# Kernel optimization log

Hardware: AMD Instinct MI355X
Metric: run time of the kernel (lower is better)

The kernel has to match this reference:

```python
import jax, jax.numpy as jnp
import numpy as np

B, S, H, F, E, K, R = 1, 1024, 1024, 4096, 8, 2, 16
SCALING = 2.0  # lora_alpha / lora_r = 32 / 16


def setup_inputs() -> dict:
    key = jax.random.key(0)
    ks = jax.random.split(key, 14)
    rnd = lambda i, shape, scale=0.02: (jax.random.normal(ks[i], shape, jnp.float32) * scale)
    return {
        "hidden_states": rnd(0, (B, S, H), 1.0),
        "noise": rnd(1, (B * S, E), 1.0),          # stands in for torch.randn_like(logits)
        "w_route": rnd(2, (H, E)),                   # gate.topkroute_linear.weight^T
        "w_noise": rnd(3, (H, E)),                   # gate.noise_linear.weight^T
        "w_gate": rnd(4, (H, F)),                    # shared mlp gate_proj
        "w_up": rnd(5, (H, F)),                      # shared mlp up_proj
        "w_down": rnd(6, (F, H)),                    # shared mlp down_proj
        "a_gate": rnd(7, (E, H, R)),                 # per-expert LoRA A/B on gate_proj
        "b_gate": rnd(8, (E, R, F)),
        "a_up": rnd(9, (E, H, R)),
        "b_up": rnd(10, (E, R, F)),
        "a_down": rnd(11, (E, F, R)),
        "b_down": rnd(12, (E, R, H)),
    }


def reference(hidden_states, noise, w_route, w_noise, w_gate, w_up, w_down,
              a_gate, b_gate, a_up, b_up, a_down, b_down):
    Bx, Sx, Hx = hidden_states.shape
    x = hidden_states.reshape(-1, Hx)                       # [T, H]
    T = x.shape[0]

    # NoisyTopkRouter
    logits = x @ w_route                                     # [T, E]
    noise_logits = x @ w_noise
    router_logits = logits + noise * jax.nn.softplus(noise_logits)

    # softmax in fp32, top-k, renormalize
    probs = jax.nn.softmax(router_logits.astype(jnp.float32), axis=-1)
    rw, sel = jax.lax.top_k(probs, K)                        # [T, K]
    rw = rw / rw.sum(axis=-1, keepdims=True)
    rw = rw.astype(x.dtype)

    # dense per-(token, expert) combine weights (equiv. to the gather/index_add loop)
    wdense = jnp.zeros((T, E), x.dtype).at[jnp.arange(T)[:, None], sel].add(rw)  # [T, E]

    # LoRA experts (Mixtral MLP shared `mlp` + per-expert low-rank adapters), vectorized over E
    gate = jnp.einsum('th,hf->tf', x, w_gate)[None] + SCALING * jnp.einsum('th,ehr,erf->etf', x, a_gate, b_gate)  # [E,T,F]
    up = jnp.einsum('th,hf->tf', x, w_up)[None] + SCALING * jnp.einsum('th,ehr,erf->etf', x, a_up, b_up)          # [E,T,F]
    act = jax.nn.silu(gate) * up                                                                                   # [E,T,F]
    down = jnp.einsum('etf,fh->eth', act, w_down) + SCALING * jnp.einsum('etf,efr,erh->eth', act, a_down, b_down)  # [E,T,H]

    out = jnp.einsum('te,eth->th', wdense, down)             # scatter-add combine
    return out.reshape(Bx, Sx, Hx), router_logits
```

## Files before the change

### kernel.cpp

```cpp
#include <hip/hip_runtime.h>
#include <hip/hip_bf16.h>

typedef __hip_bfloat16 bf16;
typedef __attribute__((ext_vector_type(4))) float f32x4;
typedef __attribute__((ext_vector_type(8))) __bf16 bf16x8;

#define T_TOK 1024
#define HDIM 1024
#define FDIM 4096
#define NEXP 8
#define RLORA 16
#define LSCALE 2.0f
#define N1 8448
#define N2 1152
#define SPLITK2 4
#define ACT_NCHUNK 8

__device__ inline float b2f(bf16 v) { return __bfloat162float(v); }
__device__ inline bf16 f2b(float v) { return __float2bfloat16(v); }
__device__ inline ushort f2u(float v) { return __builtin_bit_cast(ushort, __float2bfloat16(v)); }
__device__ inline float u2f(ushort v) { return __bfloat162float(__builtin_bit_cast(bf16, v)); }
__device__ inline float lo2f(unsigned w) { return __builtin_bit_cast(float, w << 16); }
__device__ inline float hi2f(unsigned w) { return __builtin_bit_cast(float, w & 0xffff0000u); }

typedef const __attribute__((address_space(1))) unsigned int* gptr_t;
typedef __attribute__((address_space(3))) unsigned int* lptr_t;
__device__ __forceinline__ void glds16(const void* g, void* l) {
    __builtin_amdgcn_global_load_lds((gptr_t)g, (lptr_t)l, 16, 0, 0);
}

__global__ __launch_bounds__(256) void router_kernel(
    const float* __restrict__ x, const float* __restrict__ noise,
    const float* __restrict__ w_route, const float* __restrict__ w_noise,
    float* __restrict__ rl_out, int* __restrict__ SEL, float* __restrict__ WTS)
{
    const int t = blockIdx.x, tid = threadIdx.x;
    const float* xr = x + t * HDIM;
    float acc[16];
#pragma unroll
    for (int j = 0; j < 16; j++) acc[j] = 0.f;
    for (int h = tid; h < HDIM; h += 256) {
        float xv = xr[h];
        const float* wr = w_route + h * NEXP;
        const float* wn = w_noise + h * NEXP;
#pragma unroll
        for (int j = 0; j < 8; j++) acc[j] += xv * wr[j];
#pragma unroll
        for (int j = 0; j < 8; j++) acc[8 + j] += xv * wn[j];
    }
#pragma unroll
    for (int j = 0; j < 16; j++) {
        for (int off = 32; off > 0; off >>= 1) acc[j] += __shfl_down(acc[j], off, 64);
    }
    __shared__ float red[4][16];
    const int wave = tid >> 6, lane = tid & 63;
    if (lane == 0) {
#pragma unroll
        for (int j = 0; j < 16; j++) red[wave][j] = acc[j];
    }
    __syncthreads();
    if (tid == 0) {
        float rl[8];
#pragma unroll
        for (int j = 0; j < 8; j++) {
            float lg = red[0][j] + red[1][j] + red[2][j] + red[3][j];
            float nl = red[0][8 + j] + red[1][8 + j] + red[2][8 + j] + red[3][8 + j];
            float sp = fmaxf(nl, 0.f) + log1pf(expf(-fabsf(nl)));
            rl[j] = lg + noise[t * NEXP + j] * sp;
            rl_out[t * NEXP + j] = rl[j];
        }
        float m = rl[0];
#pragma unroll
        for (int j = 1; j < 8; j++) m = fmaxf(m, rl[j]);
        float p[8];
#pragma unroll
        for (int j = 0; j < 8; j++) p[j] = expf(rl[j] - m);
        int i1 = 0;
#pragma unroll
        for (int j = 1; j < 8; j++) if (p[j] > p[i1]) i1 = j;
        int i2 = (i1 == 0) ? 1 : 0;
#pragma unroll
        for (int j = 0; j < 8; j++) { if (j != i1 && p[j] > p[i2]) i2 = j; }
        float w1 = p[i1] / (p[i1] + p[i2]);
        float w2 = p[i2] / (p[i1] + p[i2]);
        SEL[t * 2 + 0] = i1; SEL[t * 2 + 1] = i2;
        WTS[t * 2 + 0] = w1; WTS[t * 2 + 1] = w2;
    }
}

__device__ __forceinline__ void transpose_tile(
    const float* __restrict__ in, ushort* __restrict__ out,
    int rows, int cols, int bx, int by, int tid)
{
    __shared__ float tile[32][33];
    const int tx = tid & 31, ty = tid >> 5;
#pragma unroll
    for (int i = 0; i < 32; i += 8)
        tile[ty + i][tx] = in[(size_t)(by + ty + i) * cols + bx + tx];
    __syncthreads();
#pragma unroll
    for (int i = 0; i < 32; i += 8)
        out[(size_t)(bx + ty + i) * rows + by + tx] = f2u(tile[tx][ty + i]);
}

__global__ __launch_bounds__(256) void prep_kernel(
    const float* __restrict__ x,
    const float* __restrict__ w_gate, const float* __restrict__ w_up,
    const float* __restrict__ w_down,
    const float* __restrict__ a_gate, const float* __restrict__ a_up,
    const float* __restrict__ a_down,
    ushort* __restrict__ XB, ushort* __restrict__ WGUA, ushort* __restrict__ WDA,
    const int* __restrict__ SEL, int* __restrict__ CNT, int* __restrict__ LIST)
{
    const int bid = blockIdx.x, tid = threadIdx.x;
    if (bid < 4096) {
        transpose_tile(w_gate, WGUA, HDIM, FDIM, (bid & 127) * 32, (bid >> 7) * 32, tid);
    } else if (bid < 8192) {
        const int s = bid - 4096;
        transpose_tile(w_up, WGUA + (size_t)4096 * HDIM, HDIM, FDIM, (s & 127) * 32, (s >> 7) * 32, tid);
    } else if (bid < 12288) {
        const int s = bid - 8192;
        transpose_tile(w_down, WDA, FDIM, HDIM, (s & 31) * 32, (s >> 5) * 32, tid);
    } else if (bid < 12544) {
        const int row = bid - 12288;
        const int e = row >> 5, mat = (row >> 4) & 1, r = row & 15;
        const float* src = (mat ? a_up : a_gate) + (size_t)e * HDIM * RLORA;
        ushort* dst = WGUA + (size_t)(8192 + row) * HDIM;
        for (int h = tid; h < HDIM; h += 256) dst[h] = f2u(src[h * RLORA + r]);
    } else if (bid < 12672) {
        const int row = bid - 12544;
        const int e = row >> 4, r = row & 15;
        const float* src = a_down + (size_t)e * FDIM * RLORA;
        ushort* dst = WDA + (size_t)(1024 + row) * FDIM;
        for (int f = tid; f < FDIM; f += 256) dst[f] = f2u(src[f * RLORA + r]);
    } else if (bid < 13696) {
        const int i = (bid - 12672) * 256 + tid;
        const float4 v = *reinterpret_cast<const float4*>(x + (size_t)i * 4);
        ushort4 o;
        o.x = f2u(v.x); o.y = f2u(v.y); o.z = f2u(v.z); o.w = f2u(v.w);
        *reinterpret_cast<ushort4*>(XB + (size_t)i * 4) = o;
    } else {
        __shared__ int cnt[NEXP];
        if (tid < NEXP) cnt[tid] = 0;
        __syncthreads();
        for (int p = tid; p < 2 * T_TOK; p += 256) {
            const int e = SEL[p];
            const int idx = atomicAdd(&cnt[e], 1);
            LIST[e * 2048 + idx] = p;
        }
        __syncthreads();
        if (tid < NEXP) CNT[tid] = cnt[tid];
    }
}

template <int SPLITK>
__global__ __launch_bounds__(256) void gemm128(
    const ushort* __restrict__ A, const ushort* __restrict__ Bt,
    ushort* __restrict__ C, int M, int N, int Kd, int ny)
{
    __shared__ __align__(16) ushort sA[2][128 * 64];
    __shared__ __align__(16) ushort sB[2][128 * 64];
    const int nwg = gridDim.x;
    const int q = nwg >> 3;
    const int wg = (blockIdx.x & 7) * q + (blockIdx.x >> 3);
    const int bn0 = (wg / ny) * 128, bm0 = (wg % ny) * 128;

    const int tid = threadIdx.x;
    const int wave = tid >> 6, lane = tid & 63;
    const int wm = wave >> 1, wn = wave & 1;

    f32x4 acc[4][4];
#pragma unroll
    for (int m = 0; m < 4; m++)
#pragma unroll
        for (int n = 0; n < 4; n++) acc[m][n] = (f32x4){0.f, 0.f, 0.f, 0.f};

    const int srow = tid >> 3;
    const int sgrp8 = ((tid & 7) ^ (srow & 7)) * 8;

    const int kchunk = Kd / SPLITK;
    const int kbeg = blockIdx.z * kchunk;
    const int nt = kchunk >> 6;

#define STAGE(buf, kk)                                                              \
    {                                                                               \
        _Pragma("unroll")                                                           \
        for (int i = 0; i < 4; i++) {                                               \
            const int row = i * 32 + srow;                                          \
            glds16(A + (size_t)(bm0 + row) * Kd + (kk) + sgrp8,                     \
                   &sA[buf][i * 2048 + wave * 512]);                                \
            glds16(Bt + (size_t)(bn0 + row) * Kd + (kk) + sgrp8,                    \
                   &sB[buf][i * 2048 + wave * 512]);                                \
        }                                                                           \
    }

    STAGE(0, kbeg)
    for (int t = 0; t < nt; ++t) {
        const int cur = t & 1;
        __syncthreads();
        if (t + 1 < nt) STAGE(cur ^ 1, kbeg + (t + 1) * 64)
#pragma unroll
        for (int kk = 0; kk < 2; kk++) {
            bf16x8 af[4], bfr[4];
            const int colb = (kk * 32 + (lane >> 4) * 8) * 2;
#pragma unroll
            for (int m = 0; m < 4; m++) {
                const int row = wm * 64 + m * 16 + (lane & 15);
                af[m] = *reinterpret_cast<const bf16x8*>(
                    (const char*)sA[cur] + row * 128 + (colb ^ ((row & 7) << 4)));
            }
#pragma unroll
            for (int n = 0; n < 4; n++) {
                const int row = wn * 64 + n * 16 + (lane & 15);
                bfr[n] = *reinterpret_cast<const bf16x8*>(
                    (const char*)sB[cur] + row * 128 + (colb ^ ((row & 7) << 4)));
            }
#pragma unroll
            for (int m = 0; m < 4; m++)
#pragma unroll
                for (int n = 0; n < 4; n++)
                    acc[m][n] = __builtin_amdgcn_mfma_f32_16x16x32_bf16(af[m], bfr[n], acc[m][n], 0, 0, 0);
        }
        __syncthreads();
    }
#undef STAGE

    const size_t zoff = (size_t)blockIdx.z * M * N;
    const int rg = lane & 15, qg = lane >> 4;
#pragma unroll
    for (int m = 0; m < 4; m++) {
#pragma unroll
        for (int n = 0; n < 4; n++) {
            const int row0 = bm0 + wm * 64 + m * 16 + qg * 4;
            const int col = bn0 + wn * 64 + n * 16 + rg;
#pragma unroll
            for (int j = 0; j < 4; j++)
                C[zoff + (size_t)(row0 + j) * N + col] = f2u(acc[m][n][j]);
        }
    }
}

__global__ __launch_bounds__(256) void act3_kernel(
    const ushort* __restrict__ GU,
    const float* __restrict__ b_gate, const float* __restrict__ b_up,
    const int* __restrict__ CNT, const int* __restrict__ LIST,
    unsigned* __restrict__ ACT)
{
    const int e = blockIdx.x, chunk = blockIdx.z;
    const int tid = threadIdx.x;
    const int f = blockIdx.y * 512 + tid * 2;

    float2 bg[16], bu[16];
    {
        const float* bgp = b_gate + (size_t)e * RLORA * FDIM + f;
        const float* bup = b_up + (size_t)e * RLORA * FDIM + f;
#pragma unroll
        for (int r = 0; r < 16; r++) {
            bg[r] = *reinterpret_cast<const float2*>(bgp + (size_t)r * FDIM);
            bu[r] = *reinterpret_cast<const float2*>(bup + (size_t)r * FDIM);
        }
    }

    const int n = __builtin_amdgcn_readfirstlane(CNT[e]);
    for (int i = chunk; i < n; i += ACT_NCHUNK) {
        const int p = __builtin_amdgcn_readfirstlane(LIST[e * 2048 + i]);
        const int t = p >> 1;
        const ushort* gurow = GU + (size_t)t * N1;
        const unsigned* xap = (const unsigned*)(gurow + 8192 + e * 32);
        float xg[16], xu[16];
#pragma unroll
        for (int r = 0; r < 8; r++) {
            unsigned w = xap[r];
            xg[2 * r] = lo2f(w); xg[2 * r + 1] = hi2f(w);
        }
#pragma unroll
        for (int r = 0; r < 8; r++) {
            unsigned w = xap[8 + r];
            xu[2 * r] = lo2f(w); xu[2 * r + 1] = hi2f(w);
        }
        const unsigned gw = *(const unsigned*)(gurow + f);
        const unsigned uw = *(const unsigned*)(gurow + 4096 + f);
        float lg0 = 0.f, lg1 = 0.f, lu0 = 0.f, lu1 = 0.f;
#pragma unroll
        for (int r = 0; r < 16; r++) {
            lg0 += xg[r] * bg[r].x;
            lg1 += xg[r] * bg[r].y;
            lu0 += xu[r] * bu[r].x;
            lu1 += xu[r] * bu[r].y;
        }
        const float gate0 = lo2f(gw) + LSCALE * lg0;
        const float gate1 = hi2f(gw) + LSCALE * lg1;
        const float up0 = lo2f(uw) + LSCALE * lu0;
        const float up1 = hi2f(uw) + LSCALE * lu1;
        const float a0 = (gate0 / (1.f + expf(-gate0))) * up0;
        const float a1 = (gate1 / (1.f + expf(-gate1))) * up1;
        ACT[((size_t)p * FDIM + f) >> 1] = (unsigned)f2u(a0) | ((unsigned)f2u(a1) << 16);
    }
}

__global__ __launch_bounds__(256) void combine2_kernel(
    const ushort* __restrict__ C2,
    const float* __restrict__ b_down, const int* __restrict__ SEL,
    const float* __restrict__ WTS, float* __restrict__ out)
{
    const int t = blockIdx.x, tid = threadIdx.x;
    const int e0 = SEL[t * 2 + 0], e1 = SEL[t * 2 + 1];
    const float w0 = WTS[t * 2 + 0], w1 = WTS[t * 2 + 1];
    __shared__ float ad0[16], ad1[16];
    if (tid < 16) {
        float v = 0.f;
#pragma unroll
        for (int z = 0; z < SPLITK2; z++)
            v += u2f(C2[((size_t)z * 2048 + 2 * t) * N2 + 1024 + e0 * 16 + tid]);
        ad0[tid] = v;
    } else if (tid < 32) {
        float v = 0.f;
#pragma unroll
        for (int z = 0; z < SPLITK2; z++)
            v += u2f(C2[((size_t)z * 2048 + 2 * t + 1) * N2 + 1024 + e1 * 16 + (tid - 16)]);
        ad1[tid - 16] = v;
    }
    __syncthreads();
    const float* B0 = b_down + (size_t)e0 * RLORA * HDIM;
    const float* B1 = b_down + (size_t)e1 * RLORA * HDIM;
    for (int h = tid; h < HDIM; h += 256) {
        float v0 = 0.f, v1 = 0.f;
#pragma unroll
        for (int z = 0; z < SPLITK2; z++) {
            v0 += u2f(C2[((size_t)z * 2048 + 2 * t) * N2 + h]);
            v1 += u2f(C2[((size_t)z * 2048 + 2 * t + 1) * N2 + h]);
        }
        float l0 = 0.f, l1 = 0.f;
#pragma unroll
        for (int r = 0; r < 16; r++) {
            l0 += ad0[r] * B0[r * HDIM + h];
            l1 += ad1[r] * B1[r * HDIM + h];
        }
        out[(size_t)t * HDIM + h] = w0 * (v0 + LSCALE * l0) + w1 * (v1 + LSCALE * l1);
    }
}

extern "C" void kernel_launch(void* const* d_in, const int* in_sizes, int n_in,
                              void* d_out, int out_size, void* d_ws, size_t ws_size,
                              hipStream_t stream) {
    (void)in_sizes; (void)n_in; (void)out_size; (void)ws_size;
    const float* x       = (const float*)d_in[0];
    const float* noise   = (const float*)d_in[1];
    const float* w_route = (const float*)d_in[2];
    const float* w_noise = (const float*)d_in[3];
    const float* w_gate  = (const float*)d_in[4];
    const float* w_up    = (const float*)d_in[5];
    const float* w_down  = (const float*)d_in[6];
    const float* a_gate  = (const float*)d_in[7];
    const float* b_gate  = (const float*)d_in[8];
    const float* a_up    = (const float*)d_in[9];
    const float* b_up    = (const float*)d_in[10];
    const float* a_down  = (const float*)d_in[11];
    const float* b_down  = (const float*)d_in[12];
    float* out    = (float*)d_out;
    float* rl_out = out + (size_t)T_TOK * HDIM;

    char* ws = (char*)d_ws;
    ushort* C2   = (ushort*)(ws);
    ushort* WGUA = (ushort*)(ws + (size_t)(19 << 20));
    bf16*   ACT  = (bf16*)(ws + (size_t)(36 << 20));
    ushort* WDA  = (ushort*)(ws + (size_t)(52 << 20));
    ushort* XB   = (ushort*)(ws + (size_t)(62 << 20));
    ushort* C1b  = (ushort*)(ws + (size_t)(64 << 20));
    int*    LIST = (int*)(ws + (size_t)(81 << 20));
    int*    CNT  = (int*)(ws + (size_t)(81 << 20) + (1 << 17));
    int*    SEL  = (int*)(ws + (size_t)(81 << 20) + (1 << 17) + 4096);
    float*  WTS  = (float*)(ws + (size_t)(81 << 20) + (1 << 17) + 16384);

    router_kernel<<<T_TOK, 256, 0, stream>>>(x, noise, w_route, w_noise, rl_out, SEL, WTS);

    prep_kernel<<<13697, 256, 0, stream>>>(x, w_gate, w_up, w_down, a_gate, a_up, a_down,
                                           XB, WGUA, WDA, SEL, CNT, LIST);

    gemm128<1><<<dim3((N1 / 128) * (T_TOK / 128), 1, 1), 256, 0, stream>>>(
        XB, WGUA, C1b, T_TOK, N1, HDIM, T_TOK / 128);

    act3_kernel<<<dim3(NEXP, FDIM / 512, ACT_NCHUNK), 256, 0, stream>>>(
        C1b, b_gate, b_up, CNT, LIST, (unsigned*)ACT);

    gemm128<SPLITK2><<<dim3((N2 / 128) * (2 * T_TOK / 128), 1, SPLITK2), 256, 0, stream>>>(
        (const ushort*)ACT, WDA, C2, 2 * T_TOK, N2, FDIM, 2 * T_TOK / 128);

    combine2_kernel<<<T_TOK, 256, 0, stream>>>(C2, b_down, SEL, WTS, out);
}
```

Baseline: 152.3 us.

## Split-K the gate/up GEMM, deepen down split-K, single-buffer LDS tiles

The gate/up GEMM is split along K into two partial outputs, which the activation kernel now sums on load. The down-projection split-K rises from 4 to 8. The GEMM drops its LDS double buffer for a single load-sync-compute loop, halving shared memory so more workgroups fit per CU. The aim is better CU fill and occupancy, at the cost of extra partial-sum traffic and less overlap between loads and MFMA work.

```diff
diff --git a/kernel.cpp b/kernel.cpp
--- a/kernel.cpp
+++ b/kernel.cpp
@@ -13,7 +13,8 @@
 #define LSCALE 2.0f
 #define N1 8448
 #define N2 1152
-#define SPLITK2 4
+#define SPLITK1 2
+#define SPLITK2 8
 #define ACT_NCHUNK 8
 
 __device__ inline float b2f(bf16 v) { return __bfloat162float(v); }
@@ -158,8 +159,8 @@
     const ushort* __restrict__ A, const ushort* __restrict__ Bt,
     ushort* __restrict__ C, int M, int N, int Kd, int ny)
 {
-    __shared__ __align__(16) ushort sA[2][128 * 64];
-    __shared__ __align__(16) ushort sB[2][128 * 64];
+    __shared__ __align__(16) ushort sA[128 * 64];
+    __shared__ __align__(16) ushort sB[128 * 64];
     const int nwg = gridDim.x;
     const int q = nwg >> 3;
     const int wg = (blockIdx.x & 7) * q + (blockIdx.x >> 3);
@@ -179,26 +180,16 @@
     const int sgrp8 = ((tid & 7) ^ (srow & 7)) * 8;
 
     const int kchunk = Kd / SPLITK;
-    const int kbeg = blockIdx.z * kchunk;
-    const int nt = kchunk >> 6;
-
-#define STAGE(buf, kk)                                                              \
-    {                                                                               \
-        _Pragma("unroll")                                                           \
-        for (int i = 0; i < 4; i++) {                                               \
-            const int row = i * 32 + srow;                                          \
-            glds16(A + (size_t)(bm0 + row) * Kd + (kk) + sgrp8,                     \
-                   &sA[buf][i * 2048 + wave * 512]);                                \
-            glds16(Bt + (size_t)(bn0 + row) * Kd + (kk) + sgrp8,                    \
-                   &sB[buf][i * 2048 + wave * 512]);                                \
-        }                                                                           \
-    }
-
-    STAGE(0, kbeg)
-    for (int t = 0; t < nt; ++t) {
-        const int cur = t & 1;
+    const int kbeg = blockIdx.z * kchunk, kend = kbeg + kchunk;
+
+    for (int k0 = kbeg; k0 < kend; k0 += 64) {
+#pragma unroll
+        for (int i = 0; i < 4; i++) {
+            const int row = i * 32 + srow;
+            glds16(A + (size_t)(bm0 + row) * Kd + k0 + sgrp8, &sA[i * 2048 + wave * 512]);
+            glds16(Bt + (size_t)(bn0 + row) * Kd + k0 + sgrp8, &sB[i * 2048 + wave * 512]);
+        }
         __syncthreads();
-        if (t + 1 < nt) STAGE(cur ^ 1, kbeg + (t + 1) * 64)
 #pragma unroll
         for (int kk = 0; kk < 2; kk++) {
             bf16x8 af[4], bfr[4];
@@ -207,13 +198,13 @@
             for (int m = 0; m < 4; m++) {
                 const int row = wm * 64 + m * 16 + (lane & 15);
                 af[m] = *reinterpret_cast<const bf16x8*>(
-                    (const char*)sA[cur] + row * 128 + (colb ^ ((row & 7) << 4)));
+                    (const char*)sA + row * 128 + (colb ^ ((row & 7) << 4)));
             }
 #pragma unroll
             for (int n = 0; n < 4; n++) {
                 const int row = wn * 64 + n * 16 + (lane & 15);
                 bfr[n] = *reinterpret_cast<const bf16x8*>(
-                    (const char*)sB[cur] + row * 128 + (colb ^ ((row & 7) << 4)));
+                    (const char*)sB + row * 128 + (colb ^ ((row & 7) << 4)));
             }
 #pragma unroll
             for (int m = 0; m < 4; m++)
@@ -223,7 +214,6 @@
         }
         __syncthreads();
     }
-#undef STAGE
 
     const size_t zoff = (size_t)blockIdx.z * M * N;
     const int rg = lane & 15, qg = lane >> 4;
@@ -265,21 +255,27 @@
     for (int i = chunk; i < n; i += ACT_NCHUNK) {
         const int p = __builtin_amdgcn_readfirstlane(LIST[e * 2048 + i]);
         const int t = p >> 1;
-        const ushort* gurow = GU + (size_t)t * N1;
-        const unsigned* xap = (const unsigned*)(gurow + 8192 + e * 32);
+        const ushort* g0 = GU + (size_t)t * N1;
+        const ushort* g1 = GU + (size_t)T_TOK * N1 + (size_t)t * N1;
+        const unsigned* xa0 = (const unsigned*)(g0 + 8192 + e * 32);
+        const unsigned* xa1 = (const unsigned*)(g1 + 8192 + e * 32);
         float xg[16], xu[16];
 #pragma unroll
         for (int r = 0; r < 8; r++) {
-            unsigned w = xap[r];
-            xg[2 * r] = lo2f(w); xg[2 * r + 1] = hi2f(w);
+            unsigned w0 = xa0[r], w1 = xa1[r];
+            xg[2 * r] = lo2f(w0) + lo2f(w1);
+            xg[2 * r + 1] = hi2f(w0) + hi2f(w1);
         }
 #pragma unroll
         for (int r = 0; r < 8; r++) {
-            unsigned w = xap[8 + r];
-            xu[2 * r] = lo2f(w); xu[2 * r + 1] = hi2f(w);
-        }
-        const unsigned gw = *(const unsigned*)(gurow + f);
-        const unsigned uw = *(const unsigned*)(gurow + 4096 + f);
+            unsigned w0 = xa0[8 + r], w1 = xa1[8 + r];
+            xu[2 * r] = lo2f(w0) + lo2f(w1);
+            xu[2 * r + 1] = hi2f(w0) + hi2f(w1);
+        }
+        const unsigned gw0 = *(const unsigned*)(g0 + f);
+        const unsigned gw1 = *(const unsigned*)(g1 + f);
+        const unsigned uw0 = *(const unsigned*)(g0 + 4096 + f);
+        const unsigned uw1 = *(const unsigned*)(g1 + 4096 + f);
         float lg0 = 0.f, lg1 = 0.f, lu0 = 0.f, lu1 = 0.f;
 #pragma unroll
         for (int r = 0; r < 16; r++) {
@@ -288,10 +284,10 @@
             lu0 += xu[r] * bu[r].x;
             lu1 += xu[r] * bu[r].y;
         }
-        const float gate0 = lo2f(gw) + LSCALE * lg0;
-        const float gate1 = hi2f(gw) + LSCALE * lg1;
-        const float up0 = lo2f(uw) + LSCALE * lu0;
-        const float up1 = hi2f(uw) + LSCALE * lu1;
+        const float gate0 = lo2f(gw0) + lo2f(gw1) + LSCALE * lg0;
+        const float gate1 = hi2f(gw0) + hi2f(gw1) + LSCALE * lg1;
+        const float up0 = lo2f(uw0) + lo2f(uw1) + LSCALE * lu0;
+        const float up1 = hi2f(uw0) + hi2f(uw1) + LSCALE * lu1;
         const float a0 = (gate0 / (1.f + expf(-gate0))) * up0;
         const float a1 = (gate1 / (1.f + expf(-gate1))) * up1;
         ACT[((size_t)p * FDIM + f) >> 1] = (unsigned)f2u(a0) | ((unsigned)f2u(a1) << 16);
@@ -361,23 +357,23 @@
     float* rl_out = out + (size_t)T_TOK * HDIM;
 
     char* ws = (char*)d_ws;
+    ushort* C1b  = (ushort*)(ws);
     ushort* C2   = (ushort*)(ws);
-    ushort* WGUA = (ushort*)(ws + (size_t)(19 << 20));
-    bf16*   ACT  = (bf16*)(ws + (size_t)(36 << 20));
-    ushort* WDA  = (ushort*)(ws + (size_t)(52 << 20));
-    ushort* XB   = (ushort*)(ws + (size_t)(62 << 20));
-    ushort* C1b  = (ushort*)(ws + (size_t)(64 << 20));
-    int*    LIST = (int*)(ws + (size_t)(81 << 20));
-    int*    CNT  = (int*)(ws + (size_t)(81 << 20) + (1 << 17));
-    int*    SEL  = (int*)(ws + (size_t)(81 << 20) + (1 << 17) + 4096);
-    float*  WTS  = (float*)(ws + (size_t)(81 << 20) + (1 << 17) + 16384);
+    ushort* WGUA = (ushort*)(ws + (size_t)(38 << 20));
+    bf16*   ACT  = (bf16*)(ws + (size_t)(55 << 20));
+    ushort* WDA  = (ushort*)(ws + (size_t)(71 << 20));
+    ushort* XB   = (ushort*)(ws + (size_t)(80 << 20));
+    int*    LIST = (int*)(ws + (size_t)(83 << 20));
+    int*    CNT  = (int*)(ws + (size_t)(83 << 20) + (1 << 17));
+    int*    SEL  = (int*)(ws + (size_t)(83 << 20) + (1 << 17) + 4096);
+    float*  WTS  = (float*)(ws + (size_t)(83 << 20) + (1 << 17) + 16384);
 
     router_kernel<<<T_TOK, 256, 0, stream>>>(x, noise, w_route, w_noise, rl_out, SEL, WTS);
 
     prep_kernel<<<13697, 256, 0, stream>>>(x, w_gate, w_up, w_down, a_gate, a_up, a_down,
                                            XB, WGUA, WDA, SEL, CNT, LIST);
 
-    gemm128<1><<<dim3((N1 / 128) * (T_TOK / 128), 1, 1), 256, 0, stream>>>(
+    gemm128<SPLITK1><<<dim3((N1 / 128) * (T_TOK / 128), 1, SPLITK1), 256, 0, stream>>>(
         XB, WGUA, C1b, T_TOK, N1, HDIM, T_TOK / 128);
 
     act3_kernel<<<dim3(NEXP, FDIM / 512, ACT_NCHUNK), 256, 0, stream>>>(
```

New measurement: 152.6 us. Within noise of the previous version (+0.1%).
